# Optimization experiments

Hardware: AMD Instinct MI355X
Metric: run time of the kernel (lower is better)

## Reference

```python
import jax, jax.numpy as jnp
import numpy as np

N_DIM = 1024   # nodes (rows of s, rows of Kweight)
IN_DIM = 1024  # nodes / feature dim (cols of s, rows of Qweight, side of Gmat)
H_DIM = 64
B = 16


def setup_inputs() -> dict:
    key = jax.random.key(0)
    k1, k2, k3, k4 = jax.random.split(key, 4)
    s = jax.random.normal(k1, (N_DIM, B, IN_DIM), dtype=jnp.float32)
    Gmat = jax.random.uniform(k2, (IN_DIM, IN_DIM), dtype=jnp.float32)
    # torch init: rand * (4/d)**0.5 - (1/d)**0.5  => U[-(1/d)**0.5, (1/d)**0.5]... kept faithful
    Qweight = jax.random.uniform(k3, (IN_DIM, H_DIM), dtype=jnp.float32) * (4.0 / IN_DIM) ** 0.5 - (1.0 / IN_DIM) ** 0.5
    Kweight = jax.random.uniform(k4, (N_DIM, H_DIM), dtype=jnp.float32) * (4.0 / N_DIM) ** 0.5 - (1.0 / N_DIM) ** 0.5
    return {"s": s, "Gmat": Gmat, "Qweight": Qweight, "Kweight": Kweight}


def reference(s, Gmat, Qweight, Kweight):
    h_dim = Qweight.shape[1]
    inv_sqrt_h = 1.0 / jnp.sqrt(jnp.float32(h_dim))
    # q: einsum('ijk,km->ijm', s, Qw).permute(1,0,2) -> (B, n, h)
    q = jnp.einsum('nbi,ih->bnh', s, Qweight)
    # k: s.permute(1,2,0) einsum Kw then permute(0,2,1) -> (B, h, i)
    k = jnp.einsum('nbi,nh->bhi', s, Kweight)
    # squared (non-softmax) attention scores: (B, n, i)
    att = jnp.square(jnp.einsum('bnh,bhi->bni', q, k) * inv_sqrt_h + 1e-9)
    # adjacency aggregation: (B, n, i) @ (i, i)
    att = jnp.einsum('bni,ij->bnj', att, Gmat)
    # row-normalize and permute back to (n, B, i)
    s_t = jnp.sum(att, axis=2, keepdims=True) + 0.001
    return (att / s_t).transpose(1, 0, 2)
```

## Files before the change

### kernel.cpp

```cpp
#include <hip/hip_runtime.h>
#include <stdint.h>

typedef unsigned short u16;
typedef unsigned int   u32;

#define N_DIM  1024
#define IN_DIM 1024
#define H_DIM  64
#define BATCH  16

typedef __bf16 bf16x8 __attribute__((ext_vector_type(8)));
typedef float  f32x4  __attribute__((ext_vector_type(4)));

__device__ inline u16 f2bf(float f) {
    union { float f; u32 u; } v; v.f = f;
    u32 u = v.u;
    return (u16)((u + 0x7fffu + ((u >> 16) & 1u)) >> 16);
}
__device__ inline u32 pack2(float a, float b) {
    return (u32)f2bf(a) | ((u32)f2bf(b) << 16);
}

__device__ inline void gl_lds16(const u16* g, u16* l) {
    __builtin_amdgcn_global_load_lds(
        (const __attribute__((address_space(1))) u32*)g,
        (__attribute__((address_space(3))) u32*)l, 16, 0, 0);
}

__global__ void prep_w(const float* __restrict__ Q, const float* __restrict__ Kw,
                       u16* __restrict__ QT, u16* __restrict__ KwT) {
    int idx = blockIdx.x * 256 + threadIdx.x;
    const float* src = (idx < 65536) ? Q : Kw;
    u16* dst = (idx < 65536) ? QT : KwT;
    int i = idx & 65535;
    int h = i >> 10;
    int n = i & 1023;
    dst[h * 1024 + n] = f2bf(src[n * 64 + h]);
}

__global__ void prep_g(const float* __restrict__ G, u16* __restrict__ Gbt,
                       float* __restrict__ Grsum) {
    __shared__ float tile[64][65];
    int i0 = blockIdx.y * 64, j0 = blockIdx.x * 64;
    int tx = threadIdx.x & 63, ty = threadIdx.x >> 6;
    for (int r = 0; r < 16; ++r) {
        int i = ty * 16 + r;
        tile[i][tx] = G[(size_t)(i0 + i) * 1024 + j0 + tx];
    }
    __syncthreads();
    for (int r = 0; r < 16; ++r) {
        int j = ty * 16 + r;
        Gbt[(size_t)(j0 + j) * 1024 + i0 + tx] = f2bf(tile[tx][j]);
    }
    if (ty == 0) {
        float sum = 0.f;
        for (int j = 0; j < 64; ++j) sum += tile[tx][j];
        atomicAdd(&Grsum[i0 + tx], sum);
    }
}

__global__ __launch_bounds__(256) void gemm_qkt(
        const float* __restrict__ s, const u16* __restrict__ QT,
        const u16* __restrict__ KwT, u16* __restrict__ qws, u16* __restrict__ ktws) {
    int z = blockIdx.z; int b = z & 15; bool isq = (z < 16);
    int m0 = blockIdx.x * 128;
    __shared__ __align__(16) u16 As[128 * 40];
    __shared__ __align__(16) u16 Bs[64 * 40];
    const u16* Bt = isq ? QT : KwT;
    u16* outp = (isq ? qws : ktws) + (size_t)b * 65536;
    int t = threadIdx.x, lane = t & 63, w = t >> 6, quad = lane >> 4, l15 = lane & 15;
    f32x4 acc[2][4] = {};
    for (int k0 = 0; k0 < 1024; k0 += 32) {
        {
            int h = t >> 2, c = (t & 3) * 8;
            uint4 v = *(const uint4*)&Bt[(size_t)h * 1024 + k0 + c];
            *(uint4*)&Bs[h * 40 + c] = v;
        }
        if (isq) {
            int r = t >> 1, c = (t & 1) * 16;
            const float* src = s + (size_t)(m0 + r) * (BATCH * IN_DIM) + (size_t)b * IN_DIM + k0 + c;
            float4 f0 = ((const float4*)src)[0];
            float4 f1 = ((const float4*)src)[1];
            float4 f2 = ((const float4*)src)[2];
            float4 f3 = ((const float4*)src)[3];
            uint4 w0 = { pack2(f0.x,f0.y), pack2(f0.z,f0.w), pack2(f1.x,f1.y), pack2(f1.z,f1.w) };
            uint4 w1 = { pack2(f2.x,f2.y), pack2(f2.z,f2.w), pack2(f3.x,f3.y), pack2(f3.z,f3.w) };
            *(uint4*)&As[r * 40 + c]     = w0;
            *(uint4*)&As[r * 40 + c + 8] = w1;
        } else {
            int nr = t >> 3, icb = (t & 7) * 4;
            const float* src = s + (size_t)(k0 + nr) * (BATCH * IN_DIM) + (size_t)b * IN_DIM + m0;
            for (int j3 = 0; j3 < 4; ++j3) {
                float4 f = *(const float4*)&src[icb + 32 * j3];
                As[(icb + 32*j3 + 0) * 40 + nr] = f2bf(f.x);
                As[(icb + 32*j3 + 1) * 40 + nr] = f2bf(f.y);
                As[(icb + 32*j3 + 2) * 40 + nr] = f2bf(f.z);
                As[(icb + 32*j3 + 3) * 40 + nr] = f2bf(f.w);
            }
        }
        __syncthreads();
        int kh = quad * 8;
        bf16x8 af[2], bfr[4];
        for (int rt = 0; rt < 2; ++rt) af[rt] = *(const bf16x8*)&As[(w*32 + rt*16 + l15) * 40 + kh];
        for (int ct = 0; ct < 4; ++ct) bfr[ct] = *(const bf16x8*)&Bs[(ct*16 + l15) * 40 + kh];
        for (int rt = 0; rt < 2; ++rt)
            for (int ct = 0; ct < 4; ++ct)
                acc[rt][ct] = __builtin_amdgcn_mfma_f32_16x16x32_bf16(af[rt], bfr[ct], acc[rt][ct], 0, 0, 0);
        __syncthreads();
    }
    for (int rt = 0; rt < 2; ++rt)
        for (int ct = 0; ct < 4; ++ct)
            for (int r = 0; r < 4; ++r) {
                int m = w * 32 + rt * 16 + quad * 4 + r;
                int n = ct * 16 + l15;
                outp[(size_t)(m0 + m) * 64 + n] = f2bf(acc[rt][ct][r]);
            }
}

__global__ __launch_bounds__(256) void gemm_fused(
        const u16* __restrict__ qws, const u16* __restrict__ ktws,
        const u16* __restrict__ Gbt, const float* __restrict__ Grsum,
        float* __restrict__ out) {
    int b = blockIdx.z;
    int n0 = blockIdx.x * 128, m0 = blockIdx.y * 128;
    const u16* qb = qws  + (size_t)b * 65536;
    const u16* kb = ktws + (size_t)b * 65536;
    __shared__ __align__(16) u16 As[128 * 40];
    __shared__ __align__(16) u16 Bs[2][128 * 32];
    __shared__ __align__(16) u16 ktc[2][32 * 72];
    __shared__ __align__(16) float Grs[1024];
    __shared__ float rs[128];
    int t = threadIdx.x, lane = t & 63, w = t >> 6, quad = lane >> 4, l15 = lane & 15;
    int ti = w & 1;
    int wm = (w >> 1) * 64, wn = (w & 1) * 64;

    ((float4*)Grs)[t] = ((const float4*)Grsum)[t];
    if (t < 128) rs[t] = 0.f;

    bf16x8 qf[4][2];
    for (int j = 0; j < 4; ++j)
        for (int kick = 0; kick < 2; ++kick)
            qf[j][kick] = *(const bf16x8*)&qb[(size_t)(m0 + wm + j*16 + l15) * 64 + kick*32 + quad*8];

    int br = t >> 2, bc = (t & 3) * 8;
    gl_lds16(Gbt + (size_t)(n0 + br) * 1024 + bc,      &Bs[0][br * 32 + bc]);
    gl_lds16(Gbt + (size_t)(n0 + br + 64) * 1024 + bc, &Bs[0][(br + 64) * 32 + bc]);
    int ir = t >> 3, ch = (t & 7) * 8;
    uint4 kreg = *(const uint4*)&kb[(size_t)ir * 64 + ch];

    f32x4 acc[4][4] = {};
    float partial[4] = {0.f, 0.f, 0.f, 0.f};

    for (int kk = 0; kk < 32; ++kk) {
        int buf = kk & 1;
        *(uint4*)&ktc[buf][ir * 72 + ch] = kreg;
        __syncthreads();
        f32x4 sacc[4] = {};
        for (int kick = 0; kick < 2; ++kick) {
            bf16x8 ktf = *(const bf16x8*)&ktc[buf][(ti*16 + l15) * 72 + kick*32 + quad*8];
            for (int j = 0; j < 4; ++j)
                sacc[j] = __builtin_amdgcn_mfma_f32_16x16x32_bf16(ktf, qf[j][kick], sacc[j], 0, 0, 0);
        }
        if (kk < 31)
            kreg = *(const uint4*)&kb[(size_t)((kk + 1) * 32 + ir) * 64 + ch];
        float4 g = *(const float4*)&Grs[kk * 32 + ti * 16 + quad * 4];
        for (int j = 0; j < 4; ++j) {
            float v0 = sacc[j][0] * 0.125f + 1e-9f; v0 *= v0;
            float v1 = sacc[j][1] * 0.125f + 1e-9f; v1 *= v1;
            float v2 = sacc[j][2] * 0.125f + 1e-9f; v2 *= v2;
            float v3 = sacc[j][3] * 0.125f + 1e-9f; v3 *= v3;
            partial[j] += v0 * g.x + v1 * g.y + v2 * g.z + v3 * g.w;
            uint2 pk = { pack2(v0, v1), pack2(v2, v3) };
            *(uint2*)&As[(wm + j*16 + l15) * 40 + ti*16 + quad*4] = pk;
        }
        __syncthreads();
        if (kk < 31) {
            gl_lds16(Gbt + (size_t)(n0 + br) * 1024 + (kk+1)*32 + bc,      &Bs[buf^1][br * 32 + bc]);
            gl_lds16(Gbt + (size_t)(n0 + br + 64) * 1024 + (kk+1)*32 + bc, &Bs[buf^1][(br + 64) * 32 + bc]);
        }
        int kh = quad * 8;
        bf16x8 af[4], bfr[4];
        for (int i = 0; i < 4; ++i) af[i]  = *(const bf16x8*)&As[(wm + i*16 + l15) * 40 + kh];
        for (int j = 0; j < 4; ++j) bfr[j] = *(const bf16x8*)&Bs[buf][(wn + j*16 + l15) * 32 + kh];
        for (int i = 0; i < 4; ++i)
            for (int j = 0; j < 4; ++j)
                acc[i][j] = __builtin_amdgcn_mfma_f32_16x16x32_bf16(af[i], bfr[j], acc[i][j], 0, 0, 0);
    }

    for (int j = 0; j < 4; ++j) {
        partial[j] += __shfl_xor(partial[j], 16, 64);
        partial[j] += __shfl_xor(partial[j], 32, 64);
    }
    if (quad == 0)
        for (int j = 0; j < 4; ++j) atomicAdd(&rs[wm + j*16 + l15], partial[j]);
    __syncthreads();
    if (t < 128) rs[t] = 1.0f / (rs[t] + 0.001f);
    __syncthreads();

    for (int i = 0; i < 4; ++i) {
        float4 rv = *(const float4*)&rs[wm + i * 16 + quad * 4];
        float rva[4] = { rv.x, rv.y, rv.z, rv.w };
        for (int r = 0; r < 4; ++r) {
            int m = m0 + wm + i * 16 + quad * 4 + r;
            float* orow = out + (size_t)m * (BATCH * IN_DIM) + (size_t)b * IN_DIM + n0;
            for (int j = 0; j < 4; ++j)
                orow[wn + j * 16 + l15] = acc[i][j][r] * rva[r];
        }
    }
}

extern "C" void kernel_launch(void* const* d_in, const int* in_sizes, int n_in,
                              void* d_out, int out_size, void* d_ws, size_t ws_size,
                              hipStream_t stream) {
    const float* s  = (const float*)d_in[0];
    const float* G  = (const float*)d_in[1];
    const float* Q  = (const float*)d_in[2];
    const float* Kw = (const float*)d_in[3];
    float* out = (float*)d_out;
    char* ws = (char*)d_ws;

    u16*   qws   = (u16*)(ws);
    u16*   ktws  = (u16*)(ws + (size_t)(2u << 20));
    u16*   Gbt   = (u16*)(ws + (size_t)(4u << 20));
    u16*   QT    = (u16*)(ws + (size_t)(6u << 20));
    u16*   KwT   = (u16*)(ws + (size_t)(6u << 20) + (128u << 10));
    float* Grsum = (float*)(ws + (size_t)(6u << 20) + (256u << 10));

    hipMemsetAsync(Grsum, 0, 1024 * sizeof(float), stream);
    prep_w<<<512, 256, 0, stream>>>(Q, Kw, QT, KwT);
    prep_g<<<dim3(16, 16), 256, 0, stream>>>(G, Gbt, Grsum);
    gemm_qkt<<<dim3(8, 1, 32), 256, 0, stream>>>(s, QT, KwT, qws, ktws);
    gemm_fused<<<dim3(8, 8, 16), 256, 0, stream>>>(qws, ktws, Gbt, Grsum, out);
}
```

Baseline: 230.0 us.

## Split-K the projection GEMM with a reduce kernel, swizzle G tiles, single-buffer K

The q/k projection GEMM now splits its 1024-long reduction into four chunks across blockIdx.y, so it launches four times as many blocks. Each chunk writes fp32 partials to workspace, and a new reduce kernel sums them and packs the result to bf16. The fused kernel XOR-swizzles the columns of the G tile in LDS to avoid bank conflicts and drops double buffering of the K chunk. bf16 packing now uses the HIP intrinsic. In exchange, the split-K adds 32MB of fp32 partial traffic and an extra kernel launch.

```diff
diff --git a/kernel.cpp b/kernel.cpp
--- a/kernel.cpp
+++ b/kernel.cpp
@@ -1,4 +1,5 @@
 #include <hip/hip_runtime.h>
+#include <hip/hip_bf16.h>
 #include <stdint.h>
 
 typedef unsigned short u16;
@@ -18,7 +19,8 @@
     return (u16)((u + 0x7fffu + ((u >> 16) & 1u)) >> 16);
 }
 __device__ inline u32 pack2(float a, float b) {
-    return (u32)f2bf(a) | ((u32)f2bf(b) << 16);
+    __hip_bfloat162 h = __float22bfloat162_rn(float2{a, b});
+    union { __hip_bfloat162 h; u32 u; } cv; cv.h = h; return cv.u;
 }
 
 __device__ inline void gl_lds16(const u16* g, u16* l) {
@@ -61,16 +63,18 @@
 
 __global__ __launch_bounds__(256) void gemm_qkt(
         const float* __restrict__ s, const u16* __restrict__ QT,
-        const u16* __restrict__ KwT, u16* __restrict__ qws, u16* __restrict__ ktws) {
+        const u16* __restrict__ KwT, float* __restrict__ part) {
     int z = blockIdx.z; int b = z & 15; bool isq = (z < 16);
+    int ks = blockIdx.y;
     int m0 = blockIdx.x * 128;
     __shared__ __align__(16) u16 As[128 * 40];
     __shared__ __align__(16) u16 Bs[64 * 40];
     const u16* Bt = isq ? QT : KwT;
-    u16* outp = (isq ? qws : ktws) + (size_t)b * 65536;
+    float* outp = part + (size_t)ks * 2097152 + (size_t)z * 65536;
     int t = threadIdx.x, lane = t & 63, w = t >> 6, quad = lane >> 4, l15 = lane & 15;
     f32x4 acc[2][4] = {};
-    for (int k0 = 0; k0 < 1024; k0 += 32) {
+    for (int kk = 0; kk < 8; ++kk) {
+        int k0 = ks * 256 + kk * 32;
         {
             int h = t >> 2, c = (t & 3) * 8;
             uint4 v = *(const uint4*)&Bt[(size_t)h * 1024 + k0 + c];
@@ -113,8 +117,21 @@
             for (int r = 0; r < 4; ++r) {
                 int m = w * 32 + rt * 16 + quad * 4 + r;
                 int n = ct * 16 + l15;
-                outp[(size_t)(m0 + m) * 64 + n] = f2bf(acc[rt][ct][r]);
+                outp[(size_t)(m0 + m) * 64 + n] = acc[rt][ct][r];
             }
+}
+
+__global__ void reduce_qkt(const float* __restrict__ part, u16* __restrict__ qkt_out) {
+    int id = blockIdx.x * 256 + threadIdx.x;
+    const float4* p = (const float4*)part;
+    float4 a = p[id];
+    float4 b1 = p[id + 524288];
+    float4 c = p[id + 1048576];
+    float4 d = p[id + 1572864];
+    a.x += b1.x + c.x + d.x; a.y += b1.y + c.y + d.y;
+    a.z += b1.z + c.z + d.z; a.w += b1.w + c.w + d.w;
+    uint2 pk = { pack2(a.x, a.y), pack2(a.z, a.w) };
+    ((uint2*)qkt_out)[id] = pk;
 }
 
 __global__ __launch_bounds__(256) void gemm_fused(
@@ -127,7 +144,7 @@
     const u16* kb = ktws + (size_t)b * 65536;
     __shared__ __align__(16) u16 As[128 * 40];
     __shared__ __align__(16) u16 Bs[2][128 * 32];
-    __shared__ __align__(16) u16 ktc[2][32 * 72];
+    __shared__ __align__(16) u16 ktc[32 * 72];
     __shared__ __align__(16) float Grs[1024];
     __shared__ float rs[128];
     int t = threadIdx.x, lane = t & 63, w = t >> 6, quad = lane >> 4, l15 = lane & 15;
@@ -143,8 +160,9 @@
             qf[j][kick] = *(const bf16x8*)&qb[(size_t)(m0 + wm + j*16 + l15) * 64 + kick*32 + quad*8];
 
     int br = t >> 2, bc = (t & 3) * 8;
-    gl_lds16(Gbt + (size_t)(n0 + br) * 1024 + bc,      &Bs[0][br * 32 + bc]);
-    gl_lds16(Gbt + (size_t)(n0 + br + 64) * 1024 + bc, &Bs[0][(br + 64) * 32 + bc]);
+    int bsw = (br & 3) * 8;
+    gl_lds16(Gbt + (size_t)(n0 + br) * 1024 + (bc ^ bsw),      &Bs[0][br * 32 + bc]);
+    gl_lds16(Gbt + (size_t)(n0 + br + 64) * 1024 + (bc ^ bsw), &Bs[0][(br + 64) * 32 + bc]);
     int ir = t >> 3, ch = (t & 7) * 8;
     uint4 kreg = *(const uint4*)&kb[(size_t)ir * 64 + ch];
 
@@ -153,11 +171,11 @@
 
     for (int kk = 0; kk < 32; ++kk) {
         int buf = kk & 1;
-        *(uint4*)&ktc[buf][ir * 72 + ch] = kreg;
+        *(uint4*)&ktc[ir * 72 + ch] = kreg;
         __syncthreads();
         f32x4 sacc[4] = {};
         for (int kick = 0; kick < 2; ++kick) {
-            bf16x8 ktf = *(const bf16x8*)&ktc[buf][(ti*16 + l15) * 72 + kick*32 + quad*8];
+            bf16x8 ktf = *(const bf16x8*)&ktc[(ti*16 + l15) * 72 + kick*32 + quad*8];
             for (int j = 0; j < 4; ++j)
                 sacc[j] = __builtin_amdgcn_mfma_f32_16x16x32_bf16(ktf, qf[j][kick], sacc[j], 0, 0, 0);
         }
@@ -175,13 +193,16 @@
         }
         __syncthreads();
         if (kk < 31) {
-            gl_lds16(Gbt + (size_t)(n0 + br) * 1024 + (kk+1)*32 + bc,      &Bs[buf^1][br * 32 + bc]);
-            gl_lds16(Gbt + (size_t)(n0 + br + 64) * 1024 + (kk+1)*32 + bc, &Bs[buf^1][(br + 64) * 32 + bc]);
+            gl_lds16(Gbt + (size_t)(n0 + br) * 1024 + (kk+1)*32 + (bc ^ bsw),      &Bs[buf^1][br * 32 + bc]);
+            gl_lds16(Gbt + (size_t)(n0 + br + 64) * 1024 + (kk+1)*32 + (bc ^ bsw), &Bs[buf^1][(br + 64) * 32 + bc]);
         }
         int kh = quad * 8;
         bf16x8 af[4], bfr[4];
         for (int i = 0; i < 4; ++i) af[i]  = *(const bf16x8*)&As[(wm + i*16 + l15) * 40 + kh];
-        for (int j = 0; j < 4; ++j) bfr[j] = *(const bf16x8*)&Bs[buf][(wn + j*16 + l15) * 32 + kh];
+        for (int j = 0; j < 4; ++j) {
+            int row = wn + j*16 + l15;
+            bfr[j] = *(const bf16x8*)&Bs[buf][row * 32 + (kh ^ ((row & 3) * 8))];
+        }
         for (int i = 0; i < 4; ++i)
             for (int j = 0; j < 4; ++j)
                 acc[i][j] = __builtin_amdgcn_mfma_f32_16x16x32_bf16(af[i], bfr[j], acc[i][j], 0, 0, 0);
@@ -219,16 +240,18 @@
     float* out = (float*)d_out;
     char* ws = (char*)d_ws;
 
-    u16*   qws   = (u16*)(ws);
-    u16*   ktws  = (u16*)(ws + (size_t)(2u << 20));
-    u16*   Gbt   = (u16*)(ws + (size_t)(4u << 20));
-    u16*   QT    = (u16*)(ws + (size_t)(6u << 20));
-    u16*   KwT   = (u16*)(ws + (size_t)(6u << 20) + (128u << 10));
-    float* Grsum = (float*)(ws + (size_t)(6u << 20) + (256u << 10));
+    float* part  = (float*)(ws);
+    u16*   qws   = (u16*)(ws + (size_t)(32u << 20));
+    u16*   ktws  = qws + (size_t)16 * 65536;
+    u16*   Gbt   = (u16*)(ws + (size_t)(36u << 20));
+    u16*   QT    = (u16*)(ws + (size_t)(38u << 20));
+    u16*   KwT   = (u16*)(ws + (size_t)(38u << 20) + (128u << 10));
+    float* Grsum = (float*)(ws + (size_t)(38u << 20) + (256u << 10));
 
     hipMemsetAsync(Grsum, 0, 1024 * sizeof(float), stream);
     prep_w<<<512, 256, 0, stream>>>(Q, Kw, QT, KwT);
     prep_g<<<dim3(16, 16), 256, 0, stream>>>(G, Gbt, Grsum);
-    gemm_qkt<<<dim3(8, 1, 32), 256, 0, stream>>>(s, QT, KwT, qws, ktws);
+    gemm_qkt<<<dim3(8, 4, 32), 256, 0, stream>>>(s, QT, KwT, part);
+    reduce_qkt<<<2048, 256, 0, stream>>>(part, qws);
     gemm_fused<<<dim3(8, 8, 16), 256, 0, stream>>>(qws, ktws, Gbt, Grsum, out);
 }
```

After: 229.8 us. About the same (-0.1%).
